# Kernel tuning notes

Hardware: AMD Instinct MI355X
Metric: run time of the kernel (lower is better)

## Reference

```python
import jax, jax.numpy as jnp
import numpy as np

DIM = 1024
NUM_EXPERTS = 8
TOP_K = 2
HIDDEN = int(DIM * 4.0 * 2 / 3)  # 2730, matches GatedMLP hidden_dim
AUX_COEF = 0.01


def setup_inputs() -> dict:
    key = jax.random.key(0)
    ks = jax.random.split(key, 5)
    B, N = 4, 2048
    x = jax.random.normal(ks[0], (B, N, DIM), dtype=jnp.float32)
    # nn.Linear weights are [out, in]; y = x @ W.T
    gate_w = jax.random.normal(ks[1], (NUM_EXPERTS, DIM), dtype=jnp.float32) * 0.02
    w1 = jax.random.normal(ks[2], (NUM_EXPERTS, HIDDEN, DIM), dtype=jnp.float32) * 0.02
    w2 = jax.random.normal(ks[3], (NUM_EXPERTS, DIM, HIDDEN), dtype=jnp.float32) * 0.02
    w3 = jax.random.normal(ks[4], (NUM_EXPERTS, HIDDEN, DIM), dtype=jnp.float32) * 0.02
    return {"x": x, "gate_w": gate_w, "w1": w1, "w2": w2, "w3": w3}


def reference(x, gate_w, w1, w2, w3):
    # Router
    logits = jnp.einsum('bnd,ed->bne', x, gate_w)            # [B,N,E]
    probs = jax.nn.softmax(logits, axis=-1)                   # [B,N,E]
    top_v, top_i = jax.lax.top_k(probs, TOP_K)                # [B,N,K]
    top_v = top_v / jnp.sum(top_v, axis=-1, keepdims=True)
    # Combine weights per expert: sum_k prob_k * 1[idx_k == e]  -> [B,N,E]
    one_hot = jax.nn.one_hot(top_i, NUM_EXPERTS, dtype=x.dtype)  # [B,N,K,E]
    combine = jnp.einsum('bnk,bnke->bne', top_v, one_hot)
    # Per-expert SwiGLU MLP (dropout is identity in eval)
    out = jnp.zeros_like(x)
    for e in range(NUM_EXPERTS):
        h = jax.nn.silu(jnp.einsum('bnd,hd->bnh', x, w1[e])) \
            * jnp.einsum('bnd,hd->bnh', x, w3[e])             # [B,N,H]
        y = jnp.einsum('bnh,dh->bnd', h, w2[e])               # [B,N,D]
        out = out + combine[..., e:e + 1] * y
    # Load-balancing aux loss
    tokens_per_expert = jnp.mean(probs, axis=(0, 1))          # [E]
    uniform = 1.0 / NUM_EXPERTS
    aux_loss = AUX_COEF * jnp.mean((tokens_per_expert - uniform) ** 2)
    return out, aux_loss
```

## Files before the change

kernel.cpp:

```cpp
#include <hip/hip_runtime.h>
#include <hip/hip_bf16.h>
#include <stdint.h>

#define DIM   1024
#define NE    8
#define HID   2730
#define HPAD  2752
#define NTOK  8192
#define CAP   8192
#define NSLOT 16384
#define MAXBLK 136

typedef __bf16 bf16x8 __attribute__((ext_vector_type(8)));
typedef float  floatx4 __attribute__((ext_vector_type(4)));

__device__ __forceinline__ unsigned short f2bf(float f) {
    union { float f; unsigned int u; } v; v.f = f;
    unsigned int u = v.u;
    unsigned int r = (u + 0x7fffu + ((u >> 16) & 1u)) >> 16;
    return (unsigned short)r;
}

__device__ __forceinline__ float bf2f(unsigned short b) {
    union { unsigned int u; float f; } v; v.u = (unsigned int)b << 16;
    return v.f;
}

__device__ __forceinline__ void gl2lds16(const void* g, void* l) {
    __builtin_amdgcn_global_load_lds((const __attribute__((address_space(1))) void*)g,
                                     (__attribute__((address_space(3))) void*)l,
                                     16, 0, 0);
}

__global__ void convert_w_kernel(const float* __restrict__ w1, const float* __restrict__ w3,
                                 const float* __restrict__ w2,
                                 unsigned short* __restrict__ w1b, unsigned short* __restrict__ w3b,
                                 unsigned short* __restrict__ w2b,
                                 int* __restrict__ counts, float* __restrict__ psum) {
    const int HALF = (NE * HID * DIM) / 4;
    const int W13  = 2 * HALF;
    int gid = blockIdx.x * 256 + threadIdx.x;
    if (blockIdx.x == 0 && threadIdx.x < 64) {
        counts[threadIdx.x & 15] = 0;
        psum[threadIdx.x & 15] = 0.f;
    }
    if (gid < W13) {
        const float* src; unsigned short* dst; int j;
        if (gid < HALF) { src = w1; dst = w1b; j = gid; }
        else            { src = w3; dst = w3b; j = gid - HALF; }
        float4 v = ((const float4*)src)[j];
        uint2 o;
        o.x = (unsigned)f2bf(v.x) | ((unsigned)f2bf(v.y) << 16);
        o.y = (unsigned)f2bf(v.z) | ((unsigned)f2bf(v.w) << 16);
        *(uint2*)(dst + (size_t)j * 4) = o;
    } else {
        int i = gid - W13;
        int r = i / 688;
        int c = (i - r * 688) * 4;
        const float* src = w2 + (size_t)r * HID;
        unsigned short q[4];
        if (c + 3 < HID) {
            float2 v0 = *(const float2*)(src + c);
            float2 v1 = *(const float2*)(src + c + 2);
            q[0] = f2bf(v0.x); q[1] = f2bf(v0.y); q[2] = f2bf(v1.x); q[3] = f2bf(v1.y);
        } else {
#pragma unroll
            for (int j = 0; j < 4; ++j) {
                int col = c + j;
                q[j] = (col < HID) ? f2bf(src[col]) : (unsigned short)0;
            }
        }
        uint2 o;
        o.x = (unsigned)q[0] | ((unsigned)q[1] << 16);
        o.y = (unsigned)q[2] | ((unsigned)q[3] << 16);
        *(uint2*)(w2b + (size_t)r * HPAD + c) = o;
    }
}

__global__ void router_kernel(const float* __restrict__ x, const float* __restrict__ gw,
                              unsigned short* __restrict__ xb,
                              int* __restrict__ toks, int* __restrict__ meta,
                              float* __restrict__ tokw,
                              int* __restrict__ counts, float* __restrict__ psum) {
    __shared__ float gws[NE * DIM];
    __shared__ float pblk[4][NE];
    int t = threadIdx.x;
    for (int i = t; i < NE * DIM; i += 256) gws[i] = gw[i];
    __syncthreads();

    int wv = t >> 6, lane = t & 63;
    int tok = blockIdx.x * 4 + wv;
    const float4* x4 = (const float4*)(x + (size_t)tok * DIM);
    uint2* xbrow = (uint2*)(xb + (size_t)tok * DIM);

    float p[NE];
#pragma unroll
    for (int e = 0; e < NE; ++e) p[e] = 0.f;
#pragma unroll
    for (int c = 0; c < 4; ++c) {
        float4 xv = x4[c * 64 + lane];
        uint2 o;
        o.x = (unsigned)f2bf(xv.x) | ((unsigned)f2bf(xv.y) << 16);
        o.y = (unsigned)f2bf(xv.z) | ((unsigned)f2bf(xv.w) << 16);
        xbrow[c * 64 + lane] = o;
#pragma unroll
        for (int e = 0; e < NE; ++e) {
            float4 gv = ((const float4*)(gws + e * DIM))[c * 64 + lane];
            p[e] += xv.x * gv.x + xv.y * gv.y + xv.z * gv.z + xv.w * gv.w;
        }
    }
#pragma unroll
    for (int e = 0; e < NE; ++e)
#pragma unroll
        for (int s = 32; s; s >>= 1) p[e] += __shfl_xor(p[e], s, 64);

    if (lane == 0) {
        float mx = p[0];
#pragma unroll
        for (int e = 1; e < NE; ++e) mx = fmaxf(mx, p[e]);
        float ex[NE], s = 0.f;
#pragma unroll
        for (int e = 0; e < NE; ++e) { ex[e] = __expf(p[e] - mx); s += ex[e]; }
        float inv = 1.f / s;
        int i1 = 0, i2 = 0; float v1 = -1.f, v2 = -1.f;
#pragma unroll
        for (int e = 0; e < NE; ++e) {
            float pe = ex[e] * inv;
            pblk[wv][e] = pe;
            if (pe > v1)      { v2 = v1; i2 = i1; v1 = pe; i1 = e; }
            else if (pe > v2) { v2 = pe; i2 = e; }
        }
        float wn = 1.f / (v1 + v2);
        int p1 = atomicAdd(&counts[i1], 1);
        toks[i1 * CAP + p1] = tok;
        meta[tok * 2]     = (i1 << 16) | p1;
        tokw[tok * 2]     = v1 * wn;
        int p2 = atomicAdd(&counts[i2], 1);
        toks[i2 * CAP + p2] = tok;
        meta[tok * 2 + 1] = (i2 << 16) | p2;
        tokw[tok * 2 + 1] = v2 * wn;
    }
    __syncthreads();
    if (t < NE) {
        float s = pblk[0][t] + pblk[1][t] + pblk[2][t] + pblk[3][t];
        atomicAdd(&psum[t], s);
    }
}

__global__ void finalize_kernel(const int* __restrict__ counts, int* __restrict__ offs,
                                const float* __restrict__ psum, float* __restrict__ aux_out,
                                int* __restrict__ blk_e, int* __restrict__ blk_m0) {
    if (threadIdx.x == 0) {
        int off = 0, nb = 0;
        for (int e = 0; e < NE; ++e) {
            offs[e] = off;
            int M = counts[e];
            off += M;
            for (int m0 = 0; m0 < M; m0 += 128) { blk_e[nb] = e; blk_m0[nb] = m0; ++nb; }
        }
        for (; nb < MAXBLK; ++nb) { blk_e[nb] = 0; blk_m0[nb] = 0x7fffffff; }
        float s = 0.f;
        for (int e = 0; e < NE; ++e) {
            float d = psum[e] * (1.f / NTOK) - (1.f / NE);
            s += d * d;
        }
        aux_out[0] = 0.01f * s * (1.f / NE);
    }
}

__global__ __launch_bounds__(256, 2) void gemm1_kernel(
    const unsigned short* __restrict__ xb,
    const unsigned short* __restrict__ w1b,
    const unsigned short* __restrict__ w3b,
    unsigned short* __restrict__ h,
    const int* __restrict__ counts, const int* __restrict__ offs,
    const int* __restrict__ toks,
    const int* __restrict__ blk_e, const int* __restrict__ blk_m0) {
    const int id  = blockIdx.y * 22 + blockIdx.x;
    const int q   = id & 7;
    const int rest = id >> 3;
    const int xp  = rest % 22;
    const int rr  = rest / 22;
    const int slot = q * 17 + rr;
    const int e  = blk_e[slot];
    const int m0 = blk_m0[slot];
    const int M  = counts[e];
    if (m0 >= M) return;
    const int n0 = xp * 128;

    __shared__ unsigned short As[128 * 64];
    __shared__ unsigned short B1s[128 * 64];
    __shared__ unsigned short B3s[128 * 64];

    const int t = threadIdx.x;
    const int rb = t >> 3;
    const int kc = ((t & 7) ^ (rb & 7)) * 8;
    const int* tl = toks + e * CAP;
    int arow[4], brow[4];
#pragma unroll
    for (int i = 0; i < 4; ++i) {
        arow[i] = tl[min(m0 + rb + i * 32, M - 1)];
        brow[i] = min(n0 + rb + i * 32, HID - 1);
    }
    const unsigned short* w1e = w1b + (size_t)e * HID * DIM;
    const unsigned short* w3e = w3b + (size_t)e * HID * DIM;

    floatx4 acc1[4][4], acc3[4][4];
#pragma unroll
    for (int a = 0; a < 4; ++a)
#pragma unroll
        for (int b = 0; b < 4; ++b) {
            acc1[a][b] = (floatx4){0.f, 0.f, 0.f, 0.f};
            acc3[a][b] = (floatx4){0.f, 0.f, 0.f, 0.f};
        }

    const int wv = t >> 6, lane = t & 63;
    const int wm = (wv & 1) * 64, wn = (wv >> 1) * 64;
    const int lr = lane & 15, lq = lane >> 4;
    const int sw = lane & 7;

    for (int k0 = 0; k0 < DIM; k0 += 64) {
#pragma unroll
        for (int i = 0; i < 4; ++i) {
            const int ldso = (i * 256 + t) * 8;
            gl2lds16(xb + (size_t)arow[i] * DIM + k0 + kc, &As[ldso]);
            gl2lds16(w1e + (size_t)brow[i] * DIM + k0 + kc, &B1s[ldso]);
            gl2lds16(w3e + (size_t)brow[i] * DIM + k0 + kc, &B3s[ldso]);
        }
        __syncthreads();
#pragma unroll
        for (int kk = 0; kk < 64; kk += 32) {
            const int pc = (((kk >> 3) + lq) ^ sw) * 8;
            bf16x8 af[4];
#pragma unroll
            for (int mi = 0; mi < 4; ++mi)
                af[mi] = *(const bf16x8*)&As[(wm + mi * 16 + lr) * 64 + pc];
#pragma unroll
            for (int ni = 0; ni < 4; ++ni) {
                bf16x8 b1 = *(const bf16x8*)&B1s[(wn + ni * 16 + lr) * 64 + pc];
                bf16x8 b3 = *(const bf16x8*)&B3s[(wn + ni * 16 + lr) * 64 + pc];
#pragma unroll
                for (int mi = 0; mi < 4; ++mi) {
                    acc1[mi][ni] = __builtin_amdgcn_mfma_f32_16x16x32_bf16(af[mi], b1, acc1[mi][ni], 0, 0, 0);
                    acc3[mi][ni] = __builtin_amdgcn_mfma_f32_16x16x32_bf16(af[mi], b3, acc3[mi][ni], 0, 0, 0);
                }
            }
        }
        __syncthreads();
    }

    const int hb = offs[e];
#pragma unroll
    for (int mi = 0; mi < 4; ++mi) {
#pragma unroll
        for (int rg = 0; rg < 4; ++rg) {
            const int gm = m0 + wm + mi * 16 + lq * 4 + rg;
            if (gm >= M) continue;
            unsigned short* hrow = h + (size_t)(hb + gm) * HPAD;
#pragma unroll
            for (int ni = 0; ni < 4; ++ni) {
                const int col = n0 + wn + ni * 16 + lr;
                if (col >= HPAD) continue;
                float z1 = acc1[mi][ni][rg];
                float z3 = acc3[mi][ni][rg];
                float hv = z1 / (1.f + __expf(-z1)) * z3;
                hrow[col] = f2bf(hv);
            }
        }
    }
}

__global__ __launch_bounds__(256, 2) void gemm2_kernel(
    const unsigned short* __restrict__ h,
    const unsigned short* __restrict__ w2b,
    unsigned short* __restrict__ yh,
    const int* __restrict__ counts, const int* __restrict__ offs,
    const int* __restrict__ blk_e, const int* __restrict__ blk_m0) {
    const int id = (blockIdx.z * MAXBLK + blockIdx.y) * 8 + blockIdx.x;
    const int q  = id & 7;
    const int rest = id >> 3;
    const int xp = rest & 7;
    const int g  = rest >> 3;
    const int G  = q * 34 + g;
    const int slot = G % MAXBLK;
    const int kh   = G / MAXBLK;
    const int e  = blk_e[slot];
    const int m0 = blk_m0[slot];
    const int M  = counts[e];
    if (m0 >= M) return;
    const int n0 = xp * 128;

    __shared__ unsigned short As[128 * 64];
    __shared__ unsigned short Bs[128 * 64];

    const int t = threadIdx.x;
    const int rb = t >> 3;
    const int kc = ((t & 7) ^ (rb & 7)) * 8;
    const int hb = offs[e];
    int arow[4], brow[4];
#pragma unroll
    for (int i = 0; i < 4; ++i) {
        arow[i] = hb + min(m0 + rb + i * 32, M - 1);
        brow[i] = n0 + rb + i * 32;
    }
    const unsigned short* w2e = w2b + (size_t)e * DIM * HPAD;

    floatx4 acc[4][4];
#pragma unroll
    for (int a = 0; a < 4; ++a)
#pragma unroll
        for (int b = 0; b < 4; ++b) acc[a][b] = (floatx4){0.f, 0.f, 0.f, 0.f};

    const int wv = t >> 6, lane = t & 63;
    const int wm = (wv & 1) * 64, wn = (wv >> 1) * 64;
    const int lr = lane & 15, lq = lane >> 4;
    const int sw = lane & 7;

    const int kbeg = kh ? 22 * 64 : 0;
    const int kend = kh ? HPAD : 22 * 64;
    for (int k0 = kbeg; k0 < kend; k0 += 64) {
#pragma unroll
        for (int i = 0; i < 4; ++i) {
            const int ldso = (i * 256 + t) * 8;
            gl2lds16(h + (size_t)arow[i] * HPAD + k0 + kc, &As[ldso]);
            gl2lds16(w2e + (size_t)brow[i] * HPAD + k0 + kc, &Bs[ldso]);
        }
        __syncthreads();
#pragma unroll
        for (int kk = 0; kk < 64; kk += 32) {
            const int pc = (((kk >> 3) + lq) ^ sw) * 8;
            bf16x8 af[4];
#pragma unroll
            for (int mi = 0; mi < 4; ++mi)
                af[mi] = *(const bf16x8*)&As[(wm + mi * 16 + lr) * 64 + pc];
#pragma unroll
            for (int ni = 0; ni < 4; ++ni) {
                bf16x8 bf = *(const bf16x8*)&Bs[(wn + ni * 16 + lr) * 64 + pc];
#pragma unroll
                for (int mi = 0; mi < 4; ++mi)
                    acc[mi][ni] = __builtin_amdgcn_mfma_f32_16x16x32_bf16(af[mi], bf, acc[mi][ni], 0, 0, 0);
            }
        }
        __syncthreads();
    }

    unsigned short* ybase = yh + (size_t)kh * NSLOT * DIM;
#pragma unroll
    for (int mi = 0; mi < 4; ++mi) {
#pragma unroll
        for (int rg = 0; rg < 4; ++rg) {
            const int gm = m0 + wm + mi * 16 + lq * 4 + rg;
            if (gm >= M) continue;
            unsigned short* yrow = ybase + (size_t)(hb + gm) * DIM;
#pragma unroll
            for (int ni = 0; ni < 4; ++ni) {
                const int col = n0 + wn + ni * 16 + lr;
                yrow[col] = f2bf(acc[mi][ni][rg]);
            }
        }
    }
}

__global__ void combine_kernel(const unsigned short* __restrict__ yh,
                               const int* __restrict__ meta,
                               const float* __restrict__ tokw,
                               const int* __restrict__ offs,
                               float* __restrict__ out) {
    const int tok = blockIdx.x;
    const int t = threadIdx.x;
    const int m0 = meta[tok * 2], m1 = meta[tok * 2 + 1];
    const float w0 = tokw[tok * 2], w1 = tokw[tok * 2 + 1];
    const size_t r0 = (size_t)(offs[m0 >> 16] + (m0 & 0xffff)) * DIM;
    const size_t r1 = (size_t)(offs[m1 >> 16] + (m1 & 0xffff)) * DIM;
    const unsigned short* p0 = yh;
    const unsigned short* p1 = yh + (size_t)NSLOT * DIM;
    uint2 a0 = ((const uint2*)(p0 + r0))[t];
    uint2 a1 = ((const uint2*)(p1 + r0))[t];
    uint2 b0 = ((const uint2*)(p0 + r1))[t];
    uint2 b1 = ((const uint2*)(p1 + r1))[t];
    float4 o;
    o.x = w0 * (bf2f(a0.x & 0xffff) + bf2f(a1.x & 0xffff)) + w1 * (bf2f(b0.x & 0xffff) + bf2f(b1.x & 0xffff));
    o.y = w0 * (bf2f(a0.x >> 16)    + bf2f(a1.x >> 16))    + w1 * (bf2f(b0.x >> 16)    + bf2f(b1.x >> 16));
    o.z = w0 * (bf2f(a0.y & 0xffff) + bf2f(a1.y & 0xffff)) + w1 * (bf2f(b0.y & 0xffff) + bf2f(b1.y & 0xffff));
    o.w = w0 * (bf2f(a0.y >> 16)    + bf2f(a1.y >> 16))    + w1 * (bf2f(b0.y >> 16)    + bf2f(b1.y >> 16));
    ((float4*)(out + (size_t)tok * DIM))[t] = o;
}

extern "C" void kernel_launch(void* const* d_in, const int* in_sizes, int n_in,
                              void* d_out, int out_size, void* d_ws, size_t ws_size,
                              hipStream_t stream) {
    const float* x  = (const float*)d_in[0];
    const float* gw = (const float*)d_in[1];
    const float* w1 = (const float*)d_in[2];
    const float* w2 = (const float*)d_in[3];
    const float* w3 = (const float*)d_in[4];
    float* out = (float*)d_out;

    char* ws = (char*)d_ws;
    size_t o = 0;
    auto alloc = [&](size_t bytes) -> void* {
        void* p = ws + o;
        o += (bytes + 255) & ~(size_t)255;
        return p;
    };
    unsigned short* xb   = (unsigned short*)alloc((size_t)NTOK * DIM * 2);
    unsigned short* w1b  = (unsigned short*)alloc((size_t)NE * HID * DIM * 2);
    unsigned short* w3b  = (unsigned short*)alloc((size_t)NE * HID * DIM * 2);
    unsigned short* w2b  = (unsigned short*)alloc((size_t)NE * DIM * HPAD * 2);
    unsigned short* hbuf = (unsigned short*)alloc((size_t)NSLOT * HPAD * 2);
    int*   toks   = (int*)alloc((size_t)NE * CAP * 4);
    int*   meta   = (int*)alloc((size_t)NTOK * 2 * 4);
    float* tokw   = (float*)alloc((size_t)NTOK * 2 * 4);
    int*   counts = (int*)alloc(256);
    float* psum   = (float*)alloc(256);
    int*   offs   = (int*)alloc(256);
    int*   blk_e  = (int*)alloc(MAXBLK * 4);
    int*   blk_m0 = (int*)alloc(MAXBLK * 4);
    if (o > ws_size) return;
    unsigned short* yh = (unsigned short*)xb;

    convert_w_kernel<<<65696, 256, 0, stream>>>(w1, w3, w2, w1b, w3b, w2b, counts, psum);
    router_kernel<<<2048, 256, 0, stream>>>(x, gw, xb, toks, meta, tokw, counts, psum);
    finalize_kernel<<<1, 64, 0, stream>>>(counts, offs, psum, out + (size_t)NTOK * DIM, blk_e, blk_m0);
    gemm1_kernel<<<dim3(22, MAXBLK, 1), 256, 0, stream>>>(xb, w1b, w3b, hbuf, counts, offs, toks, blk_e, blk_m0);
    gemm2_kernel<<<dim3(8, MAXBLK, 2), 256, 0, stream>>>(hbuf, w2b, yh, counts, offs, blk_e, blk_m0);
    combine_kernel<<<NTOK, 256, 0, stream>>>(yh, meta, tokw, offs, out);
}
```

Baseline: 794.5 us.

## Rework expert GEMMs to 256-row tiles with 4-stage async LDS pipeline

Both expert GEMM kernels move from 128x128 tiles with 256 threads and single-buffered K=64 steps to 512-thread blocks with 256-row M tiles. Each uses a 4-slot ring of K=32 chunks loaded via global_load_lds, with explicit vmcnt waits, split barriers and s_setprio around the MFMA bursts. The goal is to overlap global loads with MFMA work and to reuse each weight tile across more tokens. The block schedule packs tiles into 8 groups of 9 slots for balance, and HPAD grows to 2816 so the K split in gemm2 divides evenly. Costs are more LDS per block, higher register pressure, and more padding waste for experts whose token count is not a multiple of 256.

```diff
diff --git a/kernel.cpp b/kernel.cpp
--- a/kernel.cpp
+++ b/kernel.cpp
@@ -5,11 +5,13 @@
 #define DIM   1024
 #define NE    8
 #define HID   2730
-#define HPAD  2752
+#define HPAD  2816
 #define NTOK  8192
 #define CAP   8192
 #define NSLOT 16384
-#define MAXBLK 136
+#define MAXB  72
+#define NCH1  32
+#define NCH2  44
 
 typedef __bf16 bf16x8 __attribute__((ext_vector_type(8)));
 typedef float  floatx4 __attribute__((ext_vector_type(4)));
@@ -55,8 +57,8 @@
         *(uint2*)(dst + (size_t)j * 4) = o;
     } else {
         int i = gid - W13;
-        int r = i / 688;
-        int c = (i - r * 688) * 4;
+        int r = i / 704;
+        int c = (i - r * 704) * 4;
         const float* src = w2 + (size_t)r * HID;
         unsigned short q[4];
         if (c + 3 < HID) {
@@ -151,24 +153,34 @@
                                 const float* __restrict__ psum, float* __restrict__ aux_out,
                                 int* __restrict__ blk_e, int* __restrict__ blk_m0) {
     if (threadIdx.x == 0) {
+        int le[MAXB], lm[MAXB];
         int off = 0, nb = 0;
         for (int e = 0; e < NE; ++e) {
             offs[e] = off;
             int M = counts[e];
             off += M;
-            for (int m0 = 0; m0 < M; m0 += 128) { blk_e[nb] = e; blk_m0[nb] = m0; ++nb; }
-        }
-        for (; nb < MAXBLK; ++nb) { blk_e[nb] = 0; blk_m0[nb] = 0x7fffffff; }
-        float s = 0.f;
+            for (int m0 = 0; m0 < M; m0 += 256) { le[nb] = e; lm[nb] = m0; ++nb; }
+        }
+        int base = 0;
+        for (int q = 0; q < 8; ++q) {
+            int n_q = nb / 8 + ((q < (nb & 7)) ? 1 : 0);
+            for (int s = 0; s < 9; ++s) {
+                int p = q * 9 + s;
+                if (s < n_q) { blk_e[p] = le[base + s]; blk_m0[p] = lm[base + s]; }
+                else         { blk_e[p] = 0; blk_m0[p] = 0x7fffffff; }
+            }
+            base += n_q;
+        }
+        float sfl = 0.f;
         for (int e = 0; e < NE; ++e) {
             float d = psum[e] * (1.f / NTOK) - (1.f / NE);
-            s += d * d;
-        }
-        aux_out[0] = 0.01f * s * (1.f / NE);
-    }
-}
-
-__global__ __launch_bounds__(256, 2) void gemm1_kernel(
+            sfl += d * d;
+        }
+        aux_out[0] = 0.01f * sfl * (1.f / NE);
+    }
+}
+
+__global__ __launch_bounds__(512, 2) void gemm1_kernel(
     const unsigned short* __restrict__ xb,
     const unsigned short* __restrict__ w1b,
     const unsigned short* __restrict__ w3b,
@@ -176,134 +188,177 @@
     const int* __restrict__ counts, const int* __restrict__ offs,
     const int* __restrict__ toks,
     const int* __restrict__ blk_e, const int* __restrict__ blk_m0) {
-    const int id  = blockIdx.y * 22 + blockIdx.x;
-    const int q   = id & 7;
-    const int rest = id >> 3;
-    const int xp  = rest % 22;
-    const int rr  = rest / 22;
-    const int slot = q * 17 + rr;
+    const int id = blockIdx.x;
+    const int q  = id & 7;
+    const int k  = id >> 3;
+    const int xp = k % 22;
+    const int slot = q * 9 + k / 22;
     const int e  = blk_e[slot];
     const int m0 = blk_m0[slot];
     const int M  = counts[e];
     if (m0 >= M) return;
     const int n0 = xp * 128;
-
-    __shared__ unsigned short As[128 * 64];
-    __shared__ unsigned short B1s[128 * 64];
-    __shared__ unsigned short B3s[128 * 64];
+    const int hb = offs[e];
+
+    __shared__ unsigned short As[4][256 * 32];
+    __shared__ unsigned short B1s[4][128 * 32];
+    __shared__ unsigned short B3s[4][128 * 32];
 
     const int t = threadIdx.x;
-    const int rb = t >> 3;
-    const int kc = ((t & 7) ^ (rb & 7)) * 8;
+    const int wv = t >> 6, l = t & 63;
+    const int srow  = wv * 16 + (l >> 2);
+    const int cl    = (l & 3) ^ ((l >> 3) & 3);
+    const int stoff = wv * 512 + l * 8;
     const int* tl = toks + e * CAP;
-    int arow[4], brow[4];
-#pragma unroll
-    for (int i = 0; i < 4; ++i) {
-        arow[i] = tl[min(m0 + rb + i * 32, M - 1)];
-        brow[i] = min(n0 + rb + i * 32, HID - 1);
-    }
-    const unsigned short* w1e = w1b + (size_t)e * HID * DIM;
-    const unsigned short* w3e = w3b + (size_t)e * HID * DIM;
-
-    floatx4 acc1[4][4], acc3[4][4];
-#pragma unroll
-    for (int a = 0; a < 4; ++a)
-#pragma unroll
-        for (int b = 0; b < 4; ++b) {
+    const int ar0 = tl[min(m0 + srow, M - 1)];
+    const int ar1 = tl[min(m0 + 128 + srow, M - 1)];
+    const int br  = min(n0 + srow, HID - 1);
+    const unsigned short* ap0 = xb + (size_t)ar0 * DIM + cl * 8;
+    const unsigned short* ap1 = xb + (size_t)ar1 * DIM + cl * 8;
+    const unsigned short* bp1 = w1b + ((size_t)e * HID + br) * DIM + cl * 8;
+    const unsigned short* bp3 = w3b + ((size_t)e * HID + br) * DIM + cl * 8;
+
+    const int lq = l >> 4, lr = l & 15;
+    const int wm = (wv & 1) * 128, wn = (wv >> 1) * 32;
+    const int pc8 = (lq ^ ((lr >> 1) & 3)) * 8;
+    int aoff[8], boff[2];
+#pragma unroll
+    for (int mi = 0; mi < 8; ++mi) aoff[mi] = (wm + mi * 16 + lr) * 32 + pc8;
+#pragma unroll
+    for (int ni = 0; ni < 2; ++ni) boff[ni] = (wn + ni * 16 + lr) * 32 + pc8;
+
+    floatx4 acc1[8][2], acc3[8][2];
+#pragma unroll
+    for (int a = 0; a < 8; ++a)
+#pragma unroll
+        for (int b = 0; b < 2; ++b) {
             acc1[a][b] = (floatx4){0.f, 0.f, 0.f, 0.f};
             acc3[a][b] = (floatx4){0.f, 0.f, 0.f, 0.f};
         }
 
-    const int wv = t >> 6, lane = t & 63;
-    const int wm = (wv & 1) * 64, wn = (wv >> 1) * 64;
-    const int lr = lane & 15, lq = lane >> 4;
-    const int sw = lane & 7;
-
-    for (int k0 = 0; k0 < DIM; k0 += 64) {
-#pragma unroll
-        for (int i = 0; i < 4; ++i) {
-            const int ldso = (i * 256 + t) * 8;
-            gl2lds16(xb + (size_t)arow[i] * DIM + k0 + kc, &As[ldso]);
-            gl2lds16(w1e + (size_t)brow[i] * DIM + k0 + kc, &B1s[ldso]);
-            gl2lds16(w3e + (size_t)brow[i] * DIM + k0 + kc, &B3s[ldso]);
-        }
-        __syncthreads();
-#pragma unroll
-        for (int kk = 0; kk < 64; kk += 32) {
-            const int pc = (((kk >> 3) + lq) ^ sw) * 8;
-            bf16x8 af[4];
-#pragma unroll
-            for (int mi = 0; mi < 4; ++mi)
-                af[mi] = *(const bf16x8*)&As[(wm + mi * 16 + lr) * 64 + pc];
-#pragma unroll
-            for (int ni = 0; ni < 4; ++ni) {
-                bf16x8 b1 = *(const bf16x8*)&B1s[(wn + ni * 16 + lr) * 64 + pc];
-                bf16x8 b3 = *(const bf16x8*)&B3s[(wn + ni * 16 + lr) * 64 + pc];
-#pragma unroll
-                for (int mi = 0; mi < 4; ++mi) {
-                    acc1[mi][ni] = __builtin_amdgcn_mfma_f32_16x16x32_bf16(af[mi], b1, acc1[mi][ni], 0, 0, 0);
-                    acc3[mi][ni] = __builtin_amdgcn_mfma_f32_16x16x32_bf16(af[mi], b3, acc3[mi][ni], 0, 0, 0);
-                }
+#pragma unroll
+    for (int pc = 0; pc < 3; ++pc) {
+        gl2lds16(ap0 + pc * 32, &As[pc][stoff]);
+        gl2lds16(ap1 + pc * 32, &As[pc][4096 + stoff]);
+        gl2lds16(bp1 + pc * 32, &B1s[pc][stoff]);
+        gl2lds16(bp3 + pc * 32, &B3s[pc][stoff]);
+    }
+
+    for (int c = 0; c < NCH1; ++c) {
+        const int sl = c & 3;
+        if (c + 2 < NCH1)      asm volatile("s_waitcnt vmcnt(8)" ::: "memory");
+        else if (c + 1 < NCH1) asm volatile("s_waitcnt vmcnt(4)" ::: "memory");
+        else                   asm volatile("s_waitcnt vmcnt(0)" ::: "memory");
+        __builtin_amdgcn_s_barrier();
+        const unsigned short* Az  = As[sl];
+        const unsigned short* B1z = B1s[sl];
+        const unsigned short* B3z = B3s[sl];
+        bf16x8 af[4], bf1[2], bf3[2];
+#pragma unroll
+        for (int ni = 0; ni < 2; ++ni) {
+            bf1[ni] = *(const bf16x8*)(B1z + boff[ni]);
+            bf3[ni] = *(const bf16x8*)(B3z + boff[ni]);
+        }
+#pragma unroll
+        for (int mi = 0; mi < 4; ++mi) af[mi] = *(const bf16x8*)(Az + aoff[mi]);
+        if (c + 3 < NCH1) {
+            const int cs = c + 3, s2 = cs & 3;
+            gl2lds16(ap0 + cs * 32, &As[s2][stoff]);
+            gl2lds16(ap1 + cs * 32, &As[s2][4096 + stoff]);
+        }
+        __builtin_amdgcn_s_barrier();
+        asm volatile("s_waitcnt lgkmcnt(0)" ::: "memory");
+        __builtin_amdgcn_s_setprio(1);
+#pragma unroll
+        for (int mi = 0; mi < 4; ++mi)
+#pragma unroll
+            for (int ni = 0; ni < 2; ++ni) {
+                acc1[mi][ni] = __builtin_amdgcn_mfma_f32_16x16x32_bf16(af[mi], bf1[ni], acc1[mi][ni], 0, 0, 0);
+                acc3[mi][ni] = __builtin_amdgcn_mfma_f32_16x16x32_bf16(af[mi], bf3[ni], acc3[mi][ni], 0, 0, 0);
             }
-        }
-        __syncthreads();
-    }
-
-    const int hb = offs[e];
-#pragma unroll
-    for (int mi = 0; mi < 4; ++mi) {
+        __builtin_amdgcn_s_setprio(0);
+        __builtin_amdgcn_s_barrier();
+#pragma unroll
+        for (int mi = 0; mi < 4; ++mi) af[mi] = *(const bf16x8*)(Az + aoff[mi + 4]);
+        if (c + 3 < NCH1) {
+            const int cs = c + 3, s2 = cs & 3;
+            gl2lds16(bp1 + cs * 32, &B1s[s2][stoff]);
+            gl2lds16(bp3 + cs * 32, &B3s[s2][stoff]);
+        }
+        __builtin_amdgcn_s_barrier();
+        asm volatile("s_waitcnt lgkmcnt(0)" ::: "memory");
+        __builtin_amdgcn_s_setprio(1);
+#pragma unroll
+        for (int mi = 0; mi < 4; ++mi)
+#pragma unroll
+            for (int ni = 0; ni < 2; ++ni) {
+                acc1[mi + 4][ni] = __builtin_amdgcn_mfma_f32_16x16x32_bf16(af[mi], bf1[ni], acc1[mi + 4][ni], 0, 0, 0);
+                acc3[mi + 4][ni] = __builtin_amdgcn_mfma_f32_16x16x32_bf16(af[mi], bf3[ni], acc3[mi + 4][ni], 0, 0, 0);
+            }
+        __builtin_amdgcn_s_setprio(0);
+    }
+
+#pragma unroll
+    for (int mi = 0; mi < 8; ++mi)
 #pragma unroll
         for (int rg = 0; rg < 4; ++rg) {
             const int gm = m0 + wm + mi * 16 + lq * 4 + rg;
             if (gm >= M) continue;
             unsigned short* hrow = h + (size_t)(hb + gm) * HPAD;
 #pragma unroll
-            for (int ni = 0; ni < 4; ++ni) {
+            for (int ni = 0; ni < 2; ++ni) {
                 const int col = n0 + wn + ni * 16 + lr;
-                if (col >= HPAD) continue;
                 float z1 = acc1[mi][ni][rg];
                 float z3 = acc3[mi][ni][rg];
-                float hv = z1 / (1.f + __expf(-z1)) * z3;
-                hrow[col] = f2bf(hv);
+                hrow[col] = f2bf(z1 / (1.f + __expf(-z1)) * z3);
             }
         }
-    }
-}
-
-__global__ __launch_bounds__(256, 2) void gemm2_kernel(
+}
+
+__global__ __launch_bounds__(512, 2) void gemm2_kernel(
     const unsigned short* __restrict__ h,
     const unsigned short* __restrict__ w2b,
     unsigned short* __restrict__ yh,
     const int* __restrict__ counts, const int* __restrict__ offs,
     const int* __restrict__ blk_e, const int* __restrict__ blk_m0) {
-    const int id = (blockIdx.z * MAXBLK + blockIdx.y) * 8 + blockIdx.x;
+    const int id = blockIdx.x;
     const int q  = id & 7;
-    const int rest = id >> 3;
-    const int xp = rest & 7;
-    const int g  = rest >> 3;
-    const int G  = q * 34 + g;
-    const int slot = G % MAXBLK;
-    const int kh   = G / MAXBLK;
+    const int k  = id >> 3;
+    const int xp = k & 7;
+    const int g  = k >> 3;
+    const int combo = q * 18 + g;
+    const int slot = combo % MAXB;
+    const int kh   = combo / MAXB;
     const int e  = blk_e[slot];
     const int m0 = blk_m0[slot];
     const int M  = counts[e];
     if (m0 >= M) return;
     const int n0 = xp * 128;
-
-    __shared__ unsigned short As[128 * 64];
-    __shared__ unsigned short Bs[128 * 64];
+    const int hb = offs[e];
+
+    __shared__ unsigned short As[4][256 * 32];
+    __shared__ unsigned short Bs[4][128 * 32];
 
     const int t = threadIdx.x;
-    const int rb = t >> 3;
-    const int kc = ((t & 7) ^ (rb & 7)) * 8;
-    const int hb = offs[e];
-    int arow[4], brow[4];
-#pragma unroll
-    for (int i = 0; i < 4; ++i) {
-        arow[i] = hb + min(m0 + rb + i * 32, M - 1);
-        brow[i] = n0 + rb + i * 32;
-    }
-    const unsigned short* w2e = w2b + (size_t)e * DIM * HPAD;
+    const int wv = t >> 6, l = t & 63;
+    const int srow  = wv * 16 + (l >> 2);
+    const int cl    = (l & 3) ^ ((l >> 3) & 3);
+    const int stoff = wv * 512 + l * 8;
+    const int ar0 = hb + min(m0 + srow, M - 1);
+    const int ar1 = hb + min(m0 + 128 + srow, M - 1);
+    const int kb  = kh * (NCH2 * 32);
+    const unsigned short* ap0 = h + (size_t)ar0 * HPAD + kb + cl * 8;
+    const unsigned short* ap1 = h + (size_t)ar1 * HPAD + kb + cl * 8;
+    const unsigned short* bp  = w2b + ((size_t)e * DIM + n0 + srow) * HPAD + kb + cl * 8;
+
+    const int lq = l >> 4, lr = l & 15;
+    const int wm = (wv >> 1) * 64, wn = (wv & 1) * 64;
+    const int pc8 = (lq ^ ((lr >> 1) & 3)) * 8;
+    int aoff[4], boff[4];
+#pragma unroll
+    for (int mi = 0; mi < 4; ++mi) aoff[mi] = (wm + mi * 16 + lr) * 32 + pc8;
+#pragma unroll
+    for (int ni = 0; ni < 4; ++ni) boff[ni] = (wn + ni * 16 + lr) * 32 + pc8;
 
     floatx4 acc[4][4];
 #pragma unroll
@@ -311,54 +366,55 @@
 #pragma unroll
         for (int b = 0; b < 4; ++b) acc[a][b] = (floatx4){0.f, 0.f, 0.f, 0.f};
 
-    const int wv = t >> 6, lane = t & 63;
-    const int wm = (wv & 1) * 64, wn = (wv >> 1) * 64;
-    const int lr = lane & 15, lq = lane >> 4;
-    const int sw = lane & 7;
-
-    const int kbeg = kh ? 22 * 64 : 0;
-    const int kend = kh ? HPAD : 22 * 64;
-    for (int k0 = kbeg; k0 < kend; k0 += 64) {
-#pragma unroll
-        for (int i = 0; i < 4; ++i) {
-            const int ldso = (i * 256 + t) * 8;
-            gl2lds16(h + (size_t)arow[i] * HPAD + k0 + kc, &As[ldso]);
-            gl2lds16(w2e + (size_t)brow[i] * HPAD + k0 + kc, &Bs[ldso]);
-        }
-        __syncthreads();
-#pragma unroll
-        for (int kk = 0; kk < 64; kk += 32) {
-            const int pc = (((kk >> 3) + lq) ^ sw) * 8;
-            bf16x8 af[4];
-#pragma unroll
-            for (int mi = 0; mi < 4; ++mi)
-                af[mi] = *(const bf16x8*)&As[(wm + mi * 16 + lr) * 64 + pc];
-#pragma unroll
-            for (int ni = 0; ni < 4; ++ni) {
-                bf16x8 bf = *(const bf16x8*)&Bs[(wn + ni * 16 + lr) * 64 + pc];
-#pragma unroll
-                for (int mi = 0; mi < 4; ++mi)
-                    acc[mi][ni] = __builtin_amdgcn_mfma_f32_16x16x32_bf16(af[mi], bf, acc[mi][ni], 0, 0, 0);
-            }
-        }
-        __syncthreads();
+#pragma unroll
+    for (int pc = 0; pc < 3; ++pc) {
+        gl2lds16(ap0 + pc * 32, &As[pc][stoff]);
+        gl2lds16(ap1 + pc * 32, &As[pc][4096 + stoff]);
+        gl2lds16(bp  + pc * 32, &Bs[pc][stoff]);
+    }
+
+    for (int c = 0; c < NCH2; ++c) {
+        const int sl = c & 3;
+        if (c + 2 < NCH2)      asm volatile("s_waitcnt vmcnt(6)" ::: "memory");
+        else if (c + 1 < NCH2) asm volatile("s_waitcnt vmcnt(3)" ::: "memory");
+        else                   asm volatile("s_waitcnt vmcnt(0)" ::: "memory");
+        __builtin_amdgcn_s_barrier();
+        const unsigned short* Az = As[sl];
+        const unsigned short* Bz = Bs[sl];
+        bf16x8 af[4], bf[4];
+#pragma unroll
+        for (int ni = 0; ni < 4; ++ni) bf[ni] = *(const bf16x8*)(Bz + boff[ni]);
+#pragma unroll
+        for (int mi = 0; mi < 4; ++mi) af[mi] = *(const bf16x8*)(Az + aoff[mi]);
+        if (c + 3 < NCH2) {
+            const int cs = c + 3, s2 = cs & 3;
+            gl2lds16(ap0 + cs * 32, &As[s2][stoff]);
+            gl2lds16(ap1 + cs * 32, &As[s2][4096 + stoff]);
+            gl2lds16(bp  + cs * 32, &Bs[s2][stoff]);
+        }
+        __builtin_amdgcn_s_barrier();
+        asm volatile("s_waitcnt lgkmcnt(0)" ::: "memory");
+        __builtin_amdgcn_s_setprio(1);
+#pragma unroll
+        for (int mi = 0; mi < 4; ++mi)
+#pragma unroll
+            for (int ni = 0; ni < 4; ++ni)
+                acc[mi][ni] = __builtin_amdgcn_mfma_f32_16x16x32_bf16(af[mi], bf[ni], acc[mi][ni], 0, 0, 0);
+        __builtin_amdgcn_s_setprio(0);
     }
 
     unsigned short* ybase = yh + (size_t)kh * NSLOT * DIM;
 #pragma unroll
-    for (int mi = 0; mi < 4; ++mi) {
+    for (int mi = 0; mi < 4; ++mi)
 #pragma unroll
         for (int rg = 0; rg < 4; ++rg) {
             const int gm = m0 + wm + mi * 16 + lq * 4 + rg;
             if (gm >= M) continue;
             unsigned short* yrow = ybase + (size_t)(hb + gm) * DIM;
 #pragma unroll
-            for (int ni = 0; ni < 4; ++ni) {
-                const int col = n0 + wn + ni * 16 + lr;
-                yrow[col] = f2bf(acc[mi][ni][rg]);
-            }
-        }
-    }
+            for (int ni = 0; ni < 4; ++ni)
+                yrow[n0 + wn + ni * 16 + lr] = f2bf(acc[mi][ni][rg]);
+        }
 }
 
 __global__ void combine_kernel(const unsigned short* __restrict__ yh,
@@ -414,15 +470,15 @@
     int*   counts = (int*)alloc(256);
     float* psum   = (float*)alloc(256);
     int*   offs   = (int*)alloc(256);
-    int*   blk_e  = (int*)alloc(MAXBLK * 4);
-    int*   blk_m0 = (int*)alloc(MAXBLK * 4);
+    int*   blk_e  = (int*)alloc(MAXB * 4);
+    int*   blk_m0 = (int*)alloc(MAXB * 4);
     if (o > ws_size) return;
     unsigned short* yh = (unsigned short*)xb;
 
-    convert_w_kernel<<<65696, 256, 0, stream>>>(w1, w3, w2, w1b, w3b, w2b, counts, psum);
+    convert_w_kernel<<<66208, 256, 0, stream>>>(w1, w3, w2, w1b, w3b, w2b, counts, psum);
     router_kernel<<<2048, 256, 0, stream>>>(x, gw, xb, toks, meta, tokw, counts, psum);
     finalize_kernel<<<1, 64, 0, stream>>>(counts, offs, psum, out + (size_t)NTOK * DIM, blk_e, blk_m0);
-    gemm1_kernel<<<dim3(22, MAXBLK, 1), 256, 0, stream>>>(xb, w1b, w3b, hbuf, counts, offs, toks, blk_e, blk_m0);
-    gemm2_kernel<<<dim3(8, MAXBLK, 2), 256, 0, stream>>>(hbuf, w2b, yh, counts, offs, blk_e, blk_m0);
+    gemm1_kernel<<<1584, 512, 0, stream>>>(xb, w1b, w3b, hbuf, counts, offs, toks, blk_e, blk_m0);
+    gemm2_kernel<<<1152, 512, 0, stream>>>(hbuf, w2b, yh, counts, offs, blk_e, blk_m0);
     combine_kernel<<<NTOK, 256, 0, stream>>>(yh, meta, tokw, offs, out);
 }
```

After: 911.2 us. 14.7% more time.

## Double-buffer LDS with K=32 chunks and async prefetch in both expert GEMMs

Applied to the files above, without the earlier changes.

Both expert GEMM kernels now use two LDS buffers of 32-wide K chunks. The next chunk's global-to-LDS loads are issued before the current chunk's MFMAs run, and a partial vmcnt wait replaces the full syncthreads, so memory latency overlaps with compute. The LDS layout gets a new rotation swizzle, the MFMA section runs at raised wave priority, and gemm2's launch bounds ask for 4 blocks per CU. The intent is to hide global-load latency. The costs are twice as many barriers per unit of K and higher register pressure under the tighter occupancy target.

```diff
diff --git a/kernel.cpp b/kernel.cpp
--- a/kernel.cpp
+++ b/kernel.cpp
@@ -10,6 +10,8 @@
 #define CAP   8192
 #define NSLOT 16384
 #define MAXBLK 136
+#define NCH1  32
+#define NCH2  43
 
 typedef __bf16 bf16x8 __attribute__((ext_vector_type(8)));
 typedef float  floatx4 __attribute__((ext_vector_type(4)));
@@ -188,22 +190,35 @@
     if (m0 >= M) return;
     const int n0 = xp * 128;
 
-    __shared__ unsigned short As[128 * 64];
-    __shared__ unsigned short B1s[128 * 64];
-    __shared__ unsigned short B3s[128 * 64];
+    __shared__ unsigned short As[2][128 * 32];
+    __shared__ unsigned short B1s[2][128 * 32];
+    __shared__ unsigned short B3s[2][128 * 32];
 
     const int t = threadIdx.x;
-    const int rb = t >> 3;
-    const int kc = ((t & 7) ^ (rb & 7)) * 8;
+    const int wv = t >> 6, l = t & 63;
+    const int r0 = wv * 16 + (l >> 2);
+    const int r1 = r0 + 64;
+    const int lc = ((l & 3) - ((l >> 3) & 3)) & 3;
+    const int st0 = (wv * 16) * 32 + l * 8;
+    const int st1 = st0 + 64 * 32;
     const int* tl = toks + e * CAP;
-    int arow[4], brow[4];
-#pragma unroll
-    for (int i = 0; i < 4; ++i) {
-        arow[i] = tl[min(m0 + rb + i * 32, M - 1)];
-        brow[i] = min(n0 + rb + i * 32, HID - 1);
-    }
+    const unsigned short* a0p = xb + (size_t)tl[min(m0 + r0, M - 1)] * DIM + lc * 8;
+    const unsigned short* a1p = xb + (size_t)tl[min(m0 + r1, M - 1)] * DIM + lc * 8;
     const unsigned short* w1e = w1b + (size_t)e * HID * DIM;
     const unsigned short* w3e = w3b + (size_t)e * HID * DIM;
+    const unsigned short* b10p = w1e + (size_t)min(n0 + r0, HID - 1) * DIM + lc * 8;
+    const unsigned short* b11p = w1e + (size_t)min(n0 + r1, HID - 1) * DIM + lc * 8;
+    const unsigned short* b30p = w3e + (size_t)min(n0 + r0, HID - 1) * DIM + lc * 8;
+    const unsigned short* b31p = w3e + (size_t)min(n0 + r1, HID - 1) * DIM + lc * 8;
+
+    const int lq = l >> 4, lr = l & 15;
+    const int wm = (wv & 1) * 64, wn = (wv >> 1) * 64;
+    const int phys = (lq + ((lr >> 1) & 3)) & 3;
+    int aoff[4], boff[4];
+#pragma unroll
+    for (int mi = 0; mi < 4; ++mi) aoff[mi] = (wm + mi * 16 + lr) * 32 + phys * 8;
+#pragma unroll
+    for (int ni = 0; ni < 4; ++ni) boff[ni] = (wn + ni * 16 + lr) * 32 + phys * 8;
 
     floatx4 acc1[4][4], acc3[4][4];
 #pragma unroll
@@ -214,39 +229,44 @@
             acc3[a][b] = (floatx4){0.f, 0.f, 0.f, 0.f};
         }
 
-    const int wv = t >> 6, lane = t & 63;
-    const int wm = (wv & 1) * 64, wn = (wv >> 1) * 64;
-    const int lr = lane & 15, lq = lane >> 4;
-    const int sw = lane & 7;
-
-    for (int k0 = 0; k0 < DIM; k0 += 64) {
-#pragma unroll
-        for (int i = 0; i < 4; ++i) {
-            const int ldso = (i * 256 + t) * 8;
-            gl2lds16(xb + (size_t)arow[i] * DIM + k0 + kc, &As[ldso]);
-            gl2lds16(w1e + (size_t)brow[i] * DIM + k0 + kc, &B1s[ldso]);
-            gl2lds16(w3e + (size_t)brow[i] * DIM + k0 + kc, &B3s[ldso]);
-        }
-        __syncthreads();
-#pragma unroll
-        for (int kk = 0; kk < 64; kk += 32) {
-            const int pc = (((kk >> 3) + lq) ^ sw) * 8;
-            bf16x8 af[4];
-#pragma unroll
-            for (int mi = 0; mi < 4; ++mi)
-                af[mi] = *(const bf16x8*)&As[(wm + mi * 16 + lr) * 64 + pc];
-#pragma unroll
-            for (int ni = 0; ni < 4; ++ni) {
-                bf16x8 b1 = *(const bf16x8*)&B1s[(wn + ni * 16 + lr) * 64 + pc];
-                bf16x8 b3 = *(const bf16x8*)&B3s[(wn + ni * 16 + lr) * 64 + pc];
-#pragma unroll
-                for (int mi = 0; mi < 4; ++mi) {
-                    acc1[mi][ni] = __builtin_amdgcn_mfma_f32_16x16x32_bf16(af[mi], b1, acc1[mi][ni], 0, 0, 0);
-                    acc3[mi][ni] = __builtin_amdgcn_mfma_f32_16x16x32_bf16(af[mi], b3, acc3[mi][ni], 0, 0, 0);
-                }
+    gl2lds16(a0p,  &As[0][st0]);  gl2lds16(a1p,  &As[0][st1]);
+    gl2lds16(b10p, &B1s[0][st0]); gl2lds16(b11p, &B1s[0][st1]);
+    gl2lds16(b30p, &B3s[0][st0]); gl2lds16(b31p, &B3s[0][st1]);
+
+    for (int c = 0; c < NCH1; ++c) {
+        const int buf = c & 1;
+        if (c + 1 < NCH1) {
+            const int ko = (c + 1) * 32;
+            const int nb = buf ^ 1;
+            gl2lds16(a0p + ko,  &As[nb][st0]);  gl2lds16(a1p + ko,  &As[nb][st1]);
+            gl2lds16(b10p + ko, &B1s[nb][st0]); gl2lds16(b11p + ko, &B1s[nb][st1]);
+            gl2lds16(b30p + ko, &B3s[nb][st0]); gl2lds16(b31p + ko, &B3s[nb][st1]);
+            asm volatile("s_waitcnt vmcnt(6)" ::: "memory");
+        } else {
+            asm volatile("s_waitcnt vmcnt(0)" ::: "memory");
+        }
+        __builtin_amdgcn_sched_barrier(0);
+        asm volatile("s_barrier" ::: "memory");
+        const unsigned short* Az  = As[buf];
+        const unsigned short* B1z = B1s[buf];
+        const unsigned short* B3z = B3s[buf];
+        bf16x8 af[4];
+#pragma unroll
+        for (int mi = 0; mi < 4; ++mi) af[mi] = *(const bf16x8*)(Az + aoff[mi]);
+        __builtin_amdgcn_s_setprio(1);
+#pragma unroll
+        for (int ni = 0; ni < 4; ++ni) {
+            bf16x8 b1 = *(const bf16x8*)(B1z + boff[ni]);
+            bf16x8 b3 = *(const bf16x8*)(B3z + boff[ni]);
+#pragma unroll
+            for (int mi = 0; mi < 4; ++mi) {
+                acc1[mi][ni] = __builtin_amdgcn_mfma_f32_16x16x32_bf16(af[mi], b1, acc1[mi][ni], 0, 0, 0);
+                acc3[mi][ni] = __builtin_amdgcn_mfma_f32_16x16x32_bf16(af[mi], b3, acc3[mi][ni], 0, 0, 0);
             }
         }
-        __syncthreads();
+        __builtin_amdgcn_s_setprio(0);
+        __builtin_amdgcn_sched_barrier(0);
+        asm volatile("s_barrier" ::: "memory");
     }
 
     const int hb = offs[e];
@@ -270,7 +290,7 @@
     }
 }
 
-__global__ __launch_bounds__(256, 2) void gemm2_kernel(
+__global__ __launch_bounds__(256, 4) void gemm2_kernel(
     const unsigned short* __restrict__ h,
     const unsigned short* __restrict__ w2b,
     unsigned short* __restrict__ yh,
@@ -289,21 +309,33 @@
     const int M  = counts[e];
     if (m0 >= M) return;
     const int n0 = xp * 128;
-
-    __shared__ unsigned short As[128 * 64];
-    __shared__ unsigned short Bs[128 * 64];
+    const int hb = offs[e];
+
+    __shared__ unsigned short As[2][128 * 32];
+    __shared__ unsigned short Bs[2][128 * 32];
 
     const int t = threadIdx.x;
-    const int rb = t >> 3;
-    const int kc = ((t & 7) ^ (rb & 7)) * 8;
-    const int hb = offs[e];
-    int arow[4], brow[4];
-#pragma unroll
-    for (int i = 0; i < 4; ++i) {
-        arow[i] = hb + min(m0 + rb + i * 32, M - 1);
-        brow[i] = n0 + rb + i * 32;
-    }
+    const int wv = t >> 6, l = t & 63;
+    const int r0 = wv * 16 + (l >> 2);
+    const int r1 = r0 + 64;
+    const int lc = ((l & 3) - ((l >> 3) & 3)) & 3;
+    const int st0 = (wv * 16) * 32 + l * 8;
+    const int st1 = st0 + 64 * 32;
+    const int kb = kh * (NCH2 * 32);
+    const unsigned short* a0p = h + (size_t)(hb + min(m0 + r0, M - 1)) * HPAD + kb + lc * 8;
+    const unsigned short* a1p = h + (size_t)(hb + min(m0 + r1, M - 1)) * HPAD + kb + lc * 8;
     const unsigned short* w2e = w2b + (size_t)e * DIM * HPAD;
+    const unsigned short* b0p = w2e + (size_t)(n0 + r0) * HPAD + kb + lc * 8;
+    const unsigned short* b1p = w2e + (size_t)(n0 + r1) * HPAD + kb + lc * 8;
+
+    const int lq = l >> 4, lr = l & 15;
+    const int wm = (wv & 1) * 64, wn = (wv >> 1) * 64;
+    const int phys = (lq + ((lr >> 1) & 3)) & 3;
+    int aoff[4], boff[4];
+#pragma unroll
+    for (int mi = 0; mi < 4; ++mi) aoff[mi] = (wm + mi * 16 + lr) * 32 + phys * 8;
+#pragma unroll
+    for (int ni = 0; ni < 4; ++ni) boff[ni] = (wn + ni * 16 + lr) * 32 + phys * 8;
 
     floatx4 acc[4][4];
 #pragma unroll
@@ -311,37 +343,38 @@
 #pragma unroll
         for (int b = 0; b < 4; ++b) acc[a][b] = (floatx4){0.f, 0.f, 0.f, 0.f};
 
-    const int wv = t >> 6, lane = t & 63;
-    const int wm = (wv & 1) * 64, wn = (wv >> 1) * 64;
-    const int lr = lane & 15, lq = lane >> 4;
-    const int sw = lane & 7;
-
-    const int kbeg = kh ? 22 * 64 : 0;
-    const int kend = kh ? HPAD : 22 * 64;
-    for (int k0 = kbeg; k0 < kend; k0 += 64) {
-#pragma unroll
-        for (int i = 0; i < 4; ++i) {
-            const int ldso = (i * 256 + t) * 8;
-            gl2lds16(h + (size_t)arow[i] * HPAD + k0 + kc, &As[ldso]);
-            gl2lds16(w2e + (size_t)brow[i] * HPAD + k0 + kc, &Bs[ldso]);
-        }
-        __syncthreads();
-#pragma unroll
-        for (int kk = 0; kk < 64; kk += 32) {
-            const int pc = (((kk >> 3) + lq) ^ sw) * 8;
-            bf16x8 af[4];
+    gl2lds16(a0p, &As[0][st0]); gl2lds16(a1p, &As[0][st1]);
+    gl2lds16(b0p, &Bs[0][st0]); gl2lds16(b1p, &Bs[0][st1]);
+
+    for (int c = 0; c < NCH2; ++c) {
+        const int buf = c & 1;
+        if (c + 1 < NCH2) {
+            const int ko = (c + 1) * 32;
+            const int nb = buf ^ 1;
+            gl2lds16(a0p + ko, &As[nb][st0]); gl2lds16(a1p + ko, &As[nb][st1]);
+            gl2lds16(b0p + ko, &Bs[nb][st0]); gl2lds16(b1p + ko, &Bs[nb][st1]);
+            asm volatile("s_waitcnt vmcnt(4)" ::: "memory");
+        } else {
+            asm volatile("s_waitcnt vmcnt(0)" ::: "memory");
+        }
+        __builtin_amdgcn_sched_barrier(0);
+        asm volatile("s_barrier" ::: "memory");
+        const unsigned short* Az = As[buf];
+        const unsigned short* Bz = Bs[buf];
+        bf16x8 af[4];
+#pragma unroll
+        for (int mi = 0; mi < 4; ++mi) af[mi] = *(const bf16x8*)(Az + aoff[mi]);
+        __builtin_amdgcn_s_setprio(1);
+#pragma unroll
+        for (int ni = 0; ni < 4; ++ni) {
+            bf16x8 bf = *(const bf16x8*)(Bz + boff[ni]);
 #pragma unroll
             for (int mi = 0; mi < 4; ++mi)
-                af[mi] = *(const bf16x8*)&As[(wm + mi * 16 + lr) * 64 + pc];
-#pragma unroll
-            for (int ni = 0; ni < 4; ++ni) {
-                bf16x8 bf = *(const bf16x8*)&Bs[(wn + ni * 16 + lr) * 64 + pc];
-#pragma unroll
-                for (int mi = 0; mi < 4; ++mi)
-                    acc[mi][ni] = __builtin_amdgcn_mfma_f32_16x16x32_bf16(af[mi], bf, acc[mi][ni], 0, 0, 0);
-            }
-        }
-        __syncthreads();
+                acc[mi][ni] = __builtin_amdgcn_mfma_f32_16x16x32_bf16(af[mi], bf, acc[mi][ni], 0, 0, 0);
+        }
+        __builtin_amdgcn_s_setprio(0);
+        __builtin_amdgcn_sched_barrier(0);
+        asm volatile("s_barrier" ::: "memory");
     }
 
     unsigned short* ybase = yh + (size_t)kh * NSLOT * DIM;
@@ -353,10 +386,8 @@
             if (gm >= M) continue;
             unsigned short* yrow = ybase + (size_t)(hb + gm) * DIM;
 #pragma unroll
-            for (int ni = 0; ni < 4; ++ni) {
-                const int col = n0 + wn + ni * 16 + lr;
-                yrow[col] = f2bf(acc[mi][ni][rg]);
-            }
+            for (int ni = 0; ni < 4; ++ni)
+                yrow[n0 + wn + ni * 16 + lr] = f2bf(acc[mi][ni][rg]);
         }
     }
 }
```

After: 835.4 us. 1.05x slower.

## Triple-buffer K=32 LDS stages in gate/up GEMM with async prefetch

Applied to the files above, without the earlier changes.

Replaces the single-buffered K=64 load/sync/compute loop in the w1/w3 expert GEMM with a three-slot ring of K=32 LDS stages. Global-to-LDS loads run two chunks ahead, using explicit vmcnt waits and one barrier per chunk, so memory traffic overlaps MFMA work. The LDS swizzle is redone for 32-wide rows. Total shared memory rises slightly, and correctness depends on the hand-written waitcnt accounting and on slot reuse being safe with only one barrier per iteration.

```diff
diff --git a/kernel.cpp b/kernel.cpp
--- a/kernel.cpp
+++ b/kernel.cpp
@@ -10,6 +10,7 @@
 #define CAP   8192
 #define NSLOT 16384
 #define MAXBLK 136
+#define NCH1  32
 
 typedef __bf16 bf16x8 __attribute__((ext_vector_type(8)));
 typedef float  floatx4 __attribute__((ext_vector_type(4)));
@@ -188,22 +189,35 @@
     if (m0 >= M) return;
     const int n0 = xp * 128;
 
-    __shared__ unsigned short As[128 * 64];
-    __shared__ unsigned short B1s[128 * 64];
-    __shared__ unsigned short B3s[128 * 64];
+    __shared__ unsigned short As[3 * 4096];
+    __shared__ unsigned short B1s[3 * 4096];
+    __shared__ unsigned short B3s[3 * 4096];
 
     const int t = threadIdx.x;
-    const int rb = t >> 3;
-    const int kc = ((t & 7) ^ (rb & 7)) * 8;
+    const int wv = t >> 6, l = t & 63;
+    const int r0 = wv * 16 + (l >> 2);
+    const int r1 = r0 + 64;
+    const int lc = ((l & 3) - ((l >> 3) & 3)) & 3;
+    const int st0 = wv * 512 + l * 8;
+    const int st1 = st0 + 2048;
     const int* tl = toks + e * CAP;
-    int arow[4], brow[4];
-#pragma unroll
-    for (int i = 0; i < 4; ++i) {
-        arow[i] = tl[min(m0 + rb + i * 32, M - 1)];
-        brow[i] = min(n0 + rb + i * 32, HID - 1);
-    }
+    const unsigned short* a0p = xb + (size_t)tl[min(m0 + r0, M - 1)] * DIM + lc * 8;
+    const unsigned short* a1p = xb + (size_t)tl[min(m0 + r1, M - 1)] * DIM + lc * 8;
     const unsigned short* w1e = w1b + (size_t)e * HID * DIM;
     const unsigned short* w3e = w3b + (size_t)e * HID * DIM;
+    const unsigned short* b10p = w1e + (size_t)min(n0 + r0, HID - 1) * DIM + lc * 8;
+    const unsigned short* b11p = w1e + (size_t)min(n0 + r1, HID - 1) * DIM + lc * 8;
+    const unsigned short* b30p = w3e + (size_t)min(n0 + r0, HID - 1) * DIM + lc * 8;
+    const unsigned short* b31p = w3e + (size_t)min(n0 + r1, HID - 1) * DIM + lc * 8;
+
+    const int lq = l >> 4, lr = l & 15;
+    const int wm = (wv & 1) * 64, wn = (wv >> 1) * 64;
+    const int phys = (lq + ((lr >> 1) & 3)) & 3;
+    int aoff[4], boff[4];
+#pragma unroll
+    for (int mi = 0; mi < 4; ++mi) aoff[mi] = (wm + mi * 16 + lr) * 32 + phys * 8;
+#pragma unroll
+    for (int ni = 0; ni < 4; ++ni) boff[ni] = (wn + ni * 16 + lr) * 32 + phys * 8;
 
     floatx4 acc1[4][4], acc3[4][4];
 #pragma unroll
@@ -214,39 +228,42 @@
             acc3[a][b] = (floatx4){0.f, 0.f, 0.f, 0.f};
         }
 
-    const int wv = t >> 6, lane = t & 63;
-    const int wm = (wv & 1) * 64, wn = (wv >> 1) * 64;
-    const int lr = lane & 15, lq = lane >> 4;
-    const int sw = lane & 7;
-
-    for (int k0 = 0; k0 < DIM; k0 += 64) {
-#pragma unroll
-        for (int i = 0; i < 4; ++i) {
-            const int ldso = (i * 256 + t) * 8;
-            gl2lds16(xb + (size_t)arow[i] * DIM + k0 + kc, &As[ldso]);
-            gl2lds16(w1e + (size_t)brow[i] * DIM + k0 + kc, &B1s[ldso]);
-            gl2lds16(w3e + (size_t)brow[i] * DIM + k0 + kc, &B3s[ldso]);
-        }
-        __syncthreads();
-#pragma unroll
-        for (int kk = 0; kk < 64; kk += 32) {
-            const int pc = (((kk >> 3) + lq) ^ sw) * 8;
-            bf16x8 af[4];
-#pragma unroll
-            for (int mi = 0; mi < 4; ++mi)
-                af[mi] = *(const bf16x8*)&As[(wm + mi * 16 + lr) * 64 + pc];
-#pragma unroll
-            for (int ni = 0; ni < 4; ++ni) {
-                bf16x8 b1 = *(const bf16x8*)&B1s[(wn + ni * 16 + lr) * 64 + pc];
-                bf16x8 b3 = *(const bf16x8*)&B3s[(wn + ni * 16 + lr) * 64 + pc];
-#pragma unroll
-                for (int mi = 0; mi < 4; ++mi) {
-                    acc1[mi][ni] = __builtin_amdgcn_mfma_f32_16x16x32_bf16(af[mi], b1, acc1[mi][ni], 0, 0, 0);
-                    acc3[mi][ni] = __builtin_amdgcn_mfma_f32_16x16x32_bf16(af[mi], b3, acc3[mi][ni], 0, 0, 0);
-                }
+#pragma unroll
+    for (int pc = 0; pc < 2; ++pc) {
+        const int ko = pc * 32, so = pc * 4096;
+        gl2lds16(a0p + ko,  &As[so + st0]);  gl2lds16(a1p + ko,  &As[so + st1]);
+        gl2lds16(b10p + ko, &B1s[so + st0]); gl2lds16(b11p + ko, &B1s[so + st1]);
+        gl2lds16(b30p + ko, &B3s[so + st0]); gl2lds16(b31p + ko, &B3s[so + st1]);
+    }
+
+    int sl_r = 0;
+    for (int c = 0; c < NCH1; ++c) {
+        if (c + 1 < NCH1) asm volatile("s_waitcnt vmcnt(6)" ::: "memory");
+        else              asm volatile("s_waitcnt vmcnt(0)" ::: "memory");
+        asm volatile("s_barrier" ::: "memory");
+        const int ro = sl_r * 4096;
+        bf16x8 af[4];
+#pragma unroll
+        for (int mi = 0; mi < 4; ++mi) af[mi] = *(const bf16x8*)&As[ro + aoff[mi]];
+        if (c + 2 < NCH1) {
+            int sl_w = sl_r + 2; if (sl_w >= 3) sl_w -= 3;
+            const int ko = (c + 2) * 32;
+            const int wo = sl_w * 4096;
+            gl2lds16(a0p + ko,  &As[wo + st0]);  gl2lds16(a1p + ko,  &As[wo + st1]);
+            gl2lds16(b10p + ko, &B1s[wo + st0]); gl2lds16(b11p + ko, &B1s[wo + st1]);
+            gl2lds16(b30p + ko, &B3s[wo + st0]); gl2lds16(b31p + ko, &B3s[wo + st1]);
+        }
+#pragma unroll
+        for (int ni = 0; ni < 4; ++ni) {
+            bf16x8 b1 = *(const bf16x8*)&B1s[ro + boff[ni]];
+            bf16x8 b3 = *(const bf16x8*)&B3s[ro + boff[ni]];
+#pragma unroll
+            for (int mi = 0; mi < 4; ++mi) {
+                acc1[mi][ni] = __builtin_amdgcn_mfma_f32_16x16x32_bf16(af[mi], b1, acc1[mi][ni], 0, 0, 0);
+                acc3[mi][ni] = __builtin_amdgcn_mfma_f32_16x16x32_bf16(af[mi], b3, acc3[mi][ni], 0, 0, 0);
             }
         }
-        __syncthreads();
+        sl_r += 1; if (sl_r == 3) sl_r = 0;
     }
 
     const int hb = offs[e];
```

Measured after the change: 841.7 us. 5.9% more time.
